# Kernel optimization log

Hardware: AMD Instinct MI355X
Metric: run time of the kernel (lower is better)

Reference implementation:

```python
import jax, jax.numpy as jnp
import numpy as np

B, N, D, H, P = 4, 512, 256, 8, 3
HD = D // H
EPS = 1e-5

def _ln(x, g, b):
    m = jnp.mean(x, axis=-1, keepdims=True)
    v = jnp.var(x, axis=-1, keepdims=True)
    return (x - m) * jax.lax.rsqrt(v + EPS) * g + b

def setup_inputs() -> dict:
    key = jax.random.key(0)
    ks = jax.random.split(key, 12)
    s = lambda *sh: 1.0 / np.sqrt(sh[0])
    return {
        "x": jax.random.normal(ks[0], (B, N, D), jnp.float32),
        "mask": jax.random.randint(ks[1], (B, N), 0, 2).astype(bool),
        "pair_feat": jax.random.normal(ks[2], (B, N, N, P), jnp.float32),
        "Wqkv": jax.random.normal(ks[3], (D, 3 * D), jnp.float32) * s(D),
        "Wout": jax.random.normal(ks[4], (D, D), jnp.float32) * s(D),
        "bout": jnp.zeros((D,), jnp.float32),
        "Wp1": jax.random.normal(ks[5], (P, D), jnp.float32) * s(P),
        "bp1": jnp.zeros((D,), jnp.float32),
        "Wp2": jax.random.normal(ks[6], (D, H), jnp.float32) * s(D),
        "bp2": jnp.zeros((H,), jnp.float32),
        "Wf1": jax.random.normal(ks[7], (D, 4 * D), jnp.float32) * s(D),
        "bf1": jnp.zeros((4 * D,), jnp.float32),
        "Wf2": jax.random.normal(ks[8], (4 * D, D), jnp.float32) * s(4 * D),
        "bf2": jnp.zeros((D,), jnp.float32),
        "g1": jnp.ones((D,), jnp.float32), "b1": jnp.zeros((D,), jnp.float32),
        "g2": jnp.ones((D,), jnp.float32), "b2": jnp.zeros((D,), jnp.float32),
    }

def reference(x, mask, pair_feat, Wqkv, Wout, bout, Wp1, bp1, Wp2, bp2,
              Wf1, bf1, Wf2, bf2, g1, b1, g2, b2):
    b_, n_, d_ = x.shape
    scale = HD ** -0.5
    qkv = x @ Wqkv                                  # [B,N,3D]
    q, k, v = jnp.split(qkv, 3, axis=-1)
    q = q.reshape(b_, n_, H, HD)
    k = k.reshape(b_, n_, H, HD)
    v = v.reshape(b_, n_, H, HD)
    logits = jnp.einsum('bihd,bjhd->bhij', q, k) * scale
    # pairwise bias MLP -> per-head bias [B,H,N,N]
    bias = jax.nn.relu(pair_feat @ Wp1 + bp1) @ Wp2 + bp2   # [B,N,N,H]
    logits = logits + jnp.transpose(bias, (0, 3, 1, 2))
    key_mask = ~mask[:, None, None, :]               # [B,1,1,N]
    logits = jnp.where(key_mask, -1e9, logits)
    attn = jax.nn.softmax(logits, axis=-1)
    out = jnp.einsum('bhij,bjhd->bihd', attn, v).reshape(b_, n_, d_)
    out = out @ Wout + bout
    x = _ln(x + out, g1, b1)
    h = jax.nn.gelu(x @ Wf1 + bf1, approximate=False) @ Wf2 + bf2
    return _ln(x + h, g2, b2)
```

## Files before the change

### kernel.cpp

```cpp
#include <hip/hip_runtime.h>
#include <hip/hip_fp16.h>
#include <math.h>

typedef unsigned short u16;
typedef short s16x8 __attribute__((ext_vector_type(8)));
typedef _Float16 f16x8 __attribute__((ext_vector_type(8)));
typedef float f32x4 __attribute__((ext_vector_type(4)));
typedef unsigned int u32x2 __attribute__((ext_vector_type(2)));

constexpr int CB = 4, CN = 512, CD = 256, CH = 8, CHD = 32;
constexpr float CEPS = 1e-5f;
constexpr int M_ROWS = CB * CN;
constexpr float QSCALE = 0.17677669529663687f;

constexpr size_t O_XB    = 0;
constexpr size_t O_QB    = 1048576;
constexpr size_t O_KB    = 2097152;
constexpr size_t O_VB    = 3145728;
constexpr size_t O_WQKVT = 4194304;
constexpr size_t O_WOUTT = O_WQKVT + 393216;
constexpr size_t O_WF1T  = O_WOUTT + 131072;
constexpr size_t O_WF2T  = O_WF1T + 524288;
constexpr size_t O_WP2T  = O_WF2T + 524288;
constexpr size_t O_PACKED= O_WP2T + 8192;
constexpr size_t O_JIDX  = O_PACKED + 4096;
constexpr size_t O_BIAS  = O_JIDX + 8192;
constexpr size_t O_AOUT  = O_BIAS + 16777216;
constexpr size_t O_H1B   = O_AOUT + 1048576;
constexpr size_t O_PRE1  = O_H1B + 4194304;
constexpr size_t O_PRE2  = O_PRE1 + 2097152;
constexpr size_t O_CNT   = O_PRE2 + 2097152;

__device__ inline u16 f2b(float f) {
  union { float f; unsigned u; } v{f};
  return (u16)((v.u + 0x7FFFu + ((v.u >> 16) & 1u)) >> 16);
}
__device__ inline float b2f(u16 b) {
  union { unsigned u; float f; } v{(unsigned)b << 16};
  return v.f;
}
__device__ inline f32x4 MFMA(s16x8 a, s16x8 b, f32x4 c) {
  return __builtin_amdgcn_mfma_f32_16x16x32_bf16(a, b, c, 0, 0, 0);
}
__device__ inline f32x4 MFMAH(f16x8 a, f16x8 b, f32x4 c) {
  return __builtin_amdgcn_mfma_f32_16x16x32_f16(a, b, c, 0, 0, 0);
}
__device__ inline unsigned cvtpk(float lo, float hi) {
  unsigned r;
  asm("v_cvt_pk_bf16_f32 %0, %1, %2" : "=v"(r) : "v"(lo), "v"(hi));
  return r;
}
__device__ inline unsigned pkmax0(unsigned a) {
  unsigned d;
  asm("v_pk_max_f16 %0, %1, 0" : "=v"(d) : "v"(a));
  return d;
}

__global__ __launch_bounds__(256) void prep_kernel(
    const float* __restrict__ x, const float* __restrict__ Wqkv,
    const float* __restrict__ Wout, const float* __restrict__ Wf1,
    const float* __restrict__ Wf2, const float* __restrict__ Wp2,
    const float* __restrict__ Wp1, const float* __restrict__ bp1,
    const unsigned char* __restrict__ maskraw,
    u16* __restrict__ xb, u16* __restrict__ wqkvt, u16* __restrict__ woutt,
    u16* __restrict__ wf1t, u16* __restrict__ wf2t, u16* __restrict__ wp2t,
    unsigned* __restrict__ packed, int* __restrict__ jidxg,
    int* __restrict__ cntg) {
  __shared__ int mode_max;
  __shared__ int mdec[2048];
  int blk = blockIdx.x, tid = threadIdx.x;
  if (blk < 256) {
    for (int t = tid; t < 512; t += 256) {
      float4 v = ((const float4*)x)[blk * 512 + t];
      u16 o0 = f2b(v.x), o1 = f2b(v.y), o2 = f2b(v.z), o3 = f2b(v.w);
      u32x2 w; w.x = (unsigned)o0 | ((unsigned)o1 << 16);
      w.y = (unsigned)o2 | ((unsigned)o3 << 16);
      *(u32x2*)(xb + (size_t)(blk * 512 + t) * 4) = w;
    }
  } else if (blk < 352) {
    int o0 = (blk - 256) * 2048;
    for (int t = tid; t < 2048; t += 256) {
      int o = o0 + t, n = o >> 8, k = o & 255;
      wqkvt[o] = f2b(Wqkv[k * 768 + n]);
    }
  } else if (blk < 384) {
    int o0 = (blk - 352) * 2048;
    for (int t = tid; t < 2048; t += 256) {
      int o = o0 + t, n = o >> 8, k = o & 255;
      woutt[o] = f2b(Wout[k * 256 + n]);
    }
  } else if (blk < 512) {
    int o0 = (blk - 384) * 2048;
    for (int t = tid; t < 2048; t += 256) {
      int o = o0 + t, n = o >> 8, k = o & 255;
      wf1t[o] = f2b(Wf1[k * 1024 + n]);
    }
  } else if (blk < 640) {
    int o0 = (blk - 512) * 2048;
    for (int t = tid; t < 2048; t += 256) {
      int o = o0 + t, n = o >> 10, k = o & 1023;
      wf2t[o] = f2b(Wf2[k * 256 + n]);
    }
  } else if (blk == 640) {
    for (int t = tid; t < 4096; t += 256) {
      int h = t >> 8, c = t & 255;
      wp2t[t] = (h < 8) ? __half_as_ushort(__float2half(Wp2[c * 8 + h])) : (u16)0;
    }
    if (tid < 128) {
      int p = tid * 2;
      unsigned w0 = (unsigned)__half_as_ushort(__float2half(Wp1[p]))
                  | ((unsigned)__half_as_ushort(__float2half(Wp1[p + 1])) << 16);
      unsigned w1 = (unsigned)__half_as_ushort(__float2half(Wp1[256 + p]))
                  | ((unsigned)__half_as_ushort(__float2half(Wp1[256 + p + 1])) << 16);
      unsigned w2 = (unsigned)__half_as_ushort(__float2half(Wp1[512 + p]))
                  | ((unsigned)__half_as_ushort(__float2half(Wp1[512 + p + 1])) << 16);
      unsigned bb = (unsigned)__half_as_ushort(__float2half(bp1[p]))
                  | ((unsigned)__half_as_ushort(__float2half(bp1[p + 1])) << 16);
      uint4 o; o.x = w0; o.y = w1; o.z = w2; o.w = bb;
      ((uint4*)packed)[tid] = o;
    }
  } else {
    if (tid == 0) mode_max = 0;
    __syncthreads();
    int lm = 0;
    for (int i = tid; i < CB*CN; i += 256)
      if ((i & 3) != 0) lm = max(lm, (int)maskraw[i]);
    atomicMax(&mode_max, lm);
    __syncthreads();
    int mv = mode_max;
    for (int i = tid; i < CB*CN; i += 256) {
      int val;
      if (mv == 0)      val = (((const int*)maskraw)[i] != 0);
      else if (mv == 1) val = (maskraw[i] != 0);
      else              val = (((const unsigned int*)maskraw)[i] != 0);
      mdec[i] = val;
    }
    __syncthreads();
    int w = tid >> 6, lane = tid & 63;
    if (w < 4) {
      int b = w, basei = 0;
      for (int c = 0; c < 8; ++c) {
        int j = c * 64 + lane;
        int m = mdec[b * 512 + j];
        unsigned long long bal = __ballot(m != 0);
        int off = __popcll(bal & ((1ull << lane) - 1ull));
        if (m) jidxg[b * 512 + basei + off] = j;
        basei += (int)__popcll(bal);
      }
      if (lane == 0) cntg[b] = basei;
      for (int p = basei + lane; p < 512; p += 64) jidxg[b * 512 + p] = 0;
    }
  }
}

__global__ __launch_bounds__(256) void qkv_pbias_kernel(
    const u16* __restrict__ A, const u16* __restrict__ Wt,
    u16* __restrict__ qb, u16* __restrict__ kb, u16* __restrict__ vb,
    const float* __restrict__ pf, const unsigned* __restrict__ packed,
    const u16* __restrict__ wp2t, const float* __restrict__ bp2,
    const int* __restrict__ jidxg, const int* __restrict__ cntg,
    u16* __restrict__ biasc) {
  __shared__ uint4 smem[1024];
  const int blk = blockIdx.x, tid = threadIdx.x;
  const int lane = tid & 63, w = tid >> 6;
  if (blk < 384) {
    u16* As = (u16*)smem;
    u16* Bs = (u16*)smem + 64 * 64;
    const int wm = w >> 1, wn = w & 1;
    const int bm = (blk / 12) * 64, bn = (blk % 12) * 64;
    f32x4 fz = {0.f, 0.f, 0.f, 0.f};
    f32x4 acc[2][2] = {{fz, fz}, {fz, fz}};
    for (int k0 = 0; k0 < 256; k0 += 64) {
#pragma unroll
      for (int t = tid; t < 512; t += 256) {
        int r = t >> 3, s = t & 7;
        s16x8 v = *(const s16x8*)(A + (size_t)(bm + r) * 256 + k0 + s * 8);
        *(s16x8*)(As + r * 64 + ((s ^ (r & 7)) << 3)) = v;
      }
#pragma unroll
      for (int t = tid; t < 512; t += 256) {
        int r = t >> 3, s = t & 7;
        s16x8 v = *(const s16x8*)(Wt + (size_t)(bn + r) * 256 + k0 + s * 8);
        *(s16x8*)(Bs + r * 64 + ((s ^ (r & 7)) << 3)) = v;
      }
      __syncthreads();
#pragma unroll
      for (int ks = 0; ks < 2; ++ks) {
        s16x8 af[2], bf[2];
#pragma unroll
        for (int mf = 0; mf < 2; ++mf) {
          int r = wm * 32 + mf * 16 + (lane & 15);
          int s = ks * 4 + (lane >> 4);
          af[mf] = *(const s16x8*)(As + r * 64 + ((s ^ (r & 7)) << 3));
        }
#pragma unroll
        for (int nf = 0; nf < 2; ++nf) {
          int r = wn * 32 + nf * 16 + (lane & 15);
          int s = ks * 4 + (lane >> 4);
          bf[nf] = *(const s16x8*)(Bs + r * 64 + ((s ^ (r & 7)) << 3));
        }
#pragma unroll
        for (int mf = 0; mf < 2; ++mf)
#pragma unroll
          for (int nf = 0; nf < 2; ++nf)
            acc[mf][nf] = MFMA(af[mf], bf[nf], acc[mf][nf]);
      }
      __syncthreads();
    }
#pragma unroll
    for (int mf = 0; mf < 2; ++mf) {
#pragma unroll
      for (int nf = 0; nf < 2; ++nf) {
#pragma unroll
        for (int r = 0; r < 4; ++r) {
          int m = bm + wm * 32 + mf * 16 + (lane >> 4) * 4 + r;
          int n = bn + wn * 32 + nf * 16 + (lane & 15);
          float v = acc[mf][nf][r];
          if (n < 256) {
            qb[(size_t)m * 256 + n] = f2b(v * QSCALE);
          } else if (n < 512) {
            kb[(size_t)m * 256 + (n - 256)] = f2b(v);
          } else {
            vb[(size_t)m * 256 + (n - 512)] = f2b(v);
          }
        }
      }
    }
  } else {
    uint4* pk = smem;
    float* pfl = (float*)(smem + 128);
    int* ji = (int*)(smem + 512);
    const int bid = blk - 384;
    const int b = bid >> 9, i = bid & 511;
    const int q = lane >> 4, hr = lane & 15;
    if (tid < 128) pk[tid] = ((const uint4*)packed)[tid];
    const float4* pfr = (const float4*)(pf + (size_t)(b * 512 + i) * 1536);
#pragma unroll
    for (int t = tid; t < 384; t += 256) ((float4*)pfl)[t] = pfr[t];
    for (int t = tid; t < 512; t += 256) ji[t] = jidxg[b * 512 + t];
    const int cnt = cntg[b];
    __syncthreads();
    __half2 f0d[8], f1d[8], f2d[8];
#pragma unroll
    for (int t = 0; t < 8; ++t) {
      int g = t * 4 + w;
      if (g * 16 < cnt) {
        int jsrc = ji[g * 16 + hr];
        f0d[t] = __float2half2_rn(pfl[jsrc * 3 + 0]);
        f1d[t] = __float2half2_rn(pfl[jsrc * 3 + 1]);
        f2d[t] = __float2half2_rn(pfl[jsrc * 3 + 2]);
      }
    }
    f32x4 fz = {0.f, 0.f, 0.f, 0.f};
    f32x4 acc[8] = {fz, fz, fz, fz, fz, fz, fz, fz};
    for (int chunk = 0; chunk < 8; ++chunk) {
      f16x8 wfrag = *(const f16x8*)(wp2t + hr * 256 + chunk * 32 + q * 8);
      int pbase = chunk * 16 + q * 4;
      __half2 w0[4], w1[4], w2[4], bb[4];
#pragma unroll
      for (int p = 0; p < 4; ++p) {
        uint4 c = pk[pbase + p];
        w0[p] = *(const __half2*)&c.x;
        w1[p] = *(const __half2*)&c.y;
        w2[p] = *(const __half2*)&c.z;
        bb[p] = *(const __half2*)&c.w;
      }
#pragma unroll
      for (int t = 0; t < 8; ++t) {
        int g = t * 4 + w;
        if (g * 16 < cnt) {
          union { unsigned u[4]; f16x8 v; } af;
#pragma unroll
          for (int p = 0; p < 4; ++p) {
            __half2 h = __hfma2(f0d[t], w0[p], bb[p]);
            h = __hfma2(f1d[t], w1[p], h);
            h = __hfma2(f2d[t], w2[p], h);
            af.u[p] = pkmax0(*(const unsigned*)&h);
          }
          acc[t] = MFMAH(af.v, wfrag, acc[t]);
        }
      }
    }
    if (hr < 8) {
      float bb = bp2[hr];
      size_t base = ((size_t)(b * 8 + hr) * 512 + i) * 512;
#pragma unroll
      for (int t = 0; t < 8; ++t) {
        int g = t * 4 + w;
        if (g * 16 < cnt) {
          int p0 = g * 16 + q * 4;
          u32x2 o;
          o.x = cvtpk(acc[t][0] + bb, acc[t][1] + bb);
          o.y = cvtpk(acc[t][2] + bb, acc[t][3] + bb);
          *(u32x2*)(biasc + base + p0) = o;
        }
      }
    }
  }
}

__global__ __launch_bounds__(512) void flash_kernel(
    const u16* __restrict__ qb, const u16* __restrict__ kb,
    const u16* __restrict__ vb, const u16* __restrict__ biasc,
    const int* __restrict__ jidxg, const int* __restrict__ cntg,
    u16* __restrict__ aout) {
  const int i0 = blockIdx.x * 64, h = blockIdx.y, b = blockIdx.z;
  const int tid = threadIdx.x;
  const int lane = tid & 63, w = tid >> 6;
  const int mf = w & 3, jhalf = w >> 2;
  __shared__ u16 qs[64 * 32];
  __shared__ u16 ksh[128 * 32];
  __shared__ u16 vs[32 * 128];
  __shared__ u16 ps[8][16 * 64];
  __shared__ float cmb[4][2][16][2];
  __shared__ int ji[512];
  for (int t = tid; t < 512; t += 512) ji[t] = jidxg[b * 512 + t];
  for (int t = tid; t < 256; t += 512) {
    int r = t >> 2, s = t & 3;
    s16x8 v = *(const s16x8*)(qb + (size_t)(b * 512 + i0 + r) * 256 + h * 32 + s * 8);
    *(s16x8*)(qs + r * 32 + ((s ^ (r & 3)) << 3)) = v;
  }
  const int cnt = cntg[b];
  __syncthreads();
  f32x4 fz = {0.f, 0.f, 0.f, 0.f};
  f32x4 oacc[2] = {fz, fz};
  float mrun[4] = {-3e38f, -3e38f, -3e38f, -3e38f};
  float lrun[4] = {0.f, 0.f, 0.f, 0.f};
  const int jj0 = jhalf * 64;
  const int il = mf * 16 + (lane >> 4) * 4;
  const u16* bbase = biasc + ((size_t)((b * 8 + h) * 512 + i0 + il)) * 512
                   + jj0 + (lane & 15);
  const int NJT = (cnt + 127) >> 7;
  for (int jc = 0; jc < NJT; ++jc) {
    int j0 = jc * 128;
    {
      int r = tid >> 2, s = tid & 3;
      int jsrc = ji[j0 + r];
      s16x8 v = *(const s16x8*)(kb + (size_t)(b * 512 + jsrc) * 256 + h * 32 + s * 8);
      *(s16x8*)(ksh + r * 32 + ((s ^ (r & 3)) << 3)) = v;
    }
    {
      int r = tid >> 2, s = tid & 3;
      int jsrc = ji[j0 + r];
      s16x8 v = *(const s16x8*)(vb + (size_t)(b * 512 + jsrc) * 256 + h * 32 + s * 8);
      int slot = r >> 3, el = r & 7;
#pragma unroll
      for (int e = 0; e < 8; ++e) {
        int d = s * 8 + e;
        vs[d * 128 + (((slot & 8) | ((slot & 7) ^ (d & 7))) << 3) + el] = (u16)v[e];
      }
    }
    u16 bvr[4][4];
#pragma unroll
    for (int jf = 0; jf < 4; ++jf)
#pragma unroll
      for (int r = 0; r < 4; ++r)
        bvr[jf][r] = bbase[(size_t)r * 512 + j0 + jf * 16];
    __syncthreads();
    int mk[4];
#pragma unroll
    for (int jf = 0; jf < 4; ++jf)
      mk[jf] = (j0 + jj0 + jf * 16 + (lane & 15)) < cnt;
    int arow = mf * 16 + (lane & 15);
    s16x8 af = *(const s16x8*)(qs + arow * 32 + (((lane >> 4) ^ (arow & 3)) << 3));
    f32x4 sm[4];
#pragma unroll
    for (int jf = 0; jf < 4; ++jf) {
      int brow = jj0 + jf * 16 + (lane & 15);
      s16x8 bfr = *(const s16x8*)(ksh + brow * 32 + (((lane >> 4) ^ (brow & 3)) << 3));
      sm[jf] = MFMA(af, bfr, fz);
    }
#pragma unroll
    for (int jf = 0; jf < 4; ++jf) {
#pragma unroll
      for (int r = 0; r < 4; ++r) {
        float sval = sm[jf][r] + b2f(bvr[jf][r]);
        sm[jf][r] = mk[jf] ? sval : -1e9f;
      }
    }
    float mx[4];
#pragma unroll
    for (int r = 0; r < 4; ++r)
      mx[r] = fmaxf(fmaxf(sm[0][r], sm[1][r]), fmaxf(sm[2][r], sm[3][r]));
#pragma unroll
    for (int d = 1; d < 16; d <<= 1)
#pragma unroll
      for (int r = 0; r < 4; ++r) mx[r] = fmaxf(mx[r], __shfl_xor(mx[r], d));
    float psl[4] = {0.f, 0.f, 0.f, 0.f};
#pragma unroll
    for (int jf = 0; jf < 4; ++jf)
#pragma unroll
      for (int r = 0; r < 4; ++r) {
        float p = __expf(sm[jf][r] - mx[r]);
        sm[jf][r] = p; psl[r] += p;
      }
#pragma unroll
    for (int d = 1; d < 16; d <<= 1)
#pragma unroll
      for (int r = 0; r < 4; ++r) psl[r] += __shfl_xor(psl[r], d);
    if ((lane & 15) == 0) {
#pragma unroll
      for (int r = 0; r < 4; ++r) {
        int row = (lane >> 4) * 4 + r;
        cmb[mf][jhalf][row][0] = mx[r];
        cmb[mf][jhalf][row][1] = psl[r];
      }
    }
    __syncthreads();
    float selfs[4];
#pragma unroll
    for (int r = 0; r < 4; ++r) {
      int row = (lane >> 4) * 4 + r;
      float omx = cmb[mf][1 - jhalf][row][0];
      float ops = cmb[mf][1 - jhalf][row][1];
      float tm = fmaxf(mx[r], omx);
      float nm = fmaxf(mrun[r], tm);
      float sc = __expf(mrun[r] - nm);
      selfs[r] = __expf(mx[r] - nm);
      float ptile = psl[r] * selfs[r] + ops * __expf(omx - nm);
      lrun[r] = lrun[r] * sc + ptile;
      mrun[r] = nm;
      oacc[0][r] *= sc; oacc[1][r] *= sc;
    }
    u16* pw = &ps[w][0];
#pragma unroll
    for (int jf = 0; jf < 4; ++jf) {
      int jcol = jf * 16 + (lane & 15);
      int slot = jcol >> 3, el = jcol & 7;
#pragma unroll
      for (int r = 0; r < 4; ++r) {
        int row = (lane >> 4) * 4 + r;
        pw[row * 64 + ((slot ^ (row & 7)) << 3) + el] = f2b(sm[jf][r] * selfs[r]);
      }
    }
#pragma unroll
    for (int kw = 0; kw < 2; ++kw) {
      int prow = lane & 15;
      s16x8 pa = *(const s16x8*)(pw + prow * 64 + (((kw * 4 + (lane >> 4)) ^ (prow & 7)) << 3));
#pragma unroll
      for (int df = 0; df < 2; ++df) {
        int drow = df * 16 + (lane & 15);
        int jcol = jj0 + kw * 32 + ((lane >> 4) << 3);
        int slot = jcol >> 3;
        s16x8 vv = *(const s16x8*)(vs + drow * 128 + (((slot & 8) | ((slot & 7) ^ (drow & 7))) << 3));
        oacc[df] = MFMA(pa, vv, oacc[df]);
      }
    }
    __syncthreads();
  }
  float* obuf = (float*)&ps[0][0];
  if (jhalf == 1) {
#pragma unroll
    for (int r = 0; r < 4; ++r) {
      int row = mf * 16 + (lane >> 4) * 4 + r;
#pragma unroll
      for (int df = 0; df < 2; ++df)
        obuf[row * 33 + df * 16 + (lane & 15)] = oacc[df][r];
    }
  }
  __syncthreads();
  if (jhalf == 0) {
#pragma unroll
    for (int r = 0; r < 4; ++r) {
      float inv = 1.0f / lrun[r];
      int row = mf * 16 + (lane >> 4) * 4 + r;
      int i = i0 + row;
#pragma unroll
      for (int df = 0; df < 2; ++df) {
        int d = df * 16 + (lane & 15);
        float o = (oacc[df][r] + obuf[row * 33 + d]) * inv;
        aout[(size_t)(b * 512 + i) * 256 + h * 32 + d] = f2b(o);
      }
    }
  }
}

__global__ __launch_bounds__(256) void mgemm_res(
    const u16* __restrict__ A, const u16* __restrict__ Wt,
    const float* __restrict__ bias, const float* __restrict__ R,
    float* __restrict__ outf, int N, int K) {
  __shared__ u16 As[32 * 64];
  __shared__ u16 Bs[64 * 64];
  const int tid = threadIdx.x;
  const int lane = tid & 63, w = tid >> 6;
  const int wm = w >> 1, wn = w & 1;
  const int bm = blockIdx.y * 32, bn = blockIdx.x * 64;
  f32x4 fz = {0.f, 0.f, 0.f, 0.f};
  f32x4 acc[2] = {fz, fz};
  for (int k0 = 0; k0 < K; k0 += 64) {
    for (int t = tid; t < 256; t += 256) {
      int r = t >> 3, s = t & 7;
      s16x8 v = *(const s16x8*)(A + (size_t)(bm + r) * K + k0 + s * 8);
      *(s16x8*)(As + r * 64 + ((s ^ (r & 7)) << 3)) = v;
    }
#pragma unroll
    for (int t = tid; t < 512; t += 256) {
      int r = t >> 3, s = t & 7;
      s16x8 v = *(const s16x8*)(Wt + (size_t)(bn + r) * K + k0 + s * 8);
      *(s16x8*)(Bs + r * 64 + ((s ^ (r & 7)) << 3)) = v;
    }
    __syncthreads();
#pragma unroll
    for (int ks = 0; ks < 2; ++ks) {
      int r = wm * 16 + (lane & 15);
      int s = ks * 4 + (lane >> 4);
      s16x8 af = *(const s16x8*)(As + r * 64 + ((s ^ (r & 7)) << 3));
#pragma unroll
      for (int nf = 0; nf < 2; ++nf) {
        int br = wn * 32 + nf * 16 + (lane & 15);
        s16x8 bf = *(const s16x8*)(Bs + br * 64 + ((s ^ (br & 7)) << 3));
        acc[nf] = MFMA(af, bf, acc[nf]);
      }
    }
    __syncthreads();
  }
#pragma unroll
  for (int nf = 0; nf < 2; ++nf) {
#pragma unroll
    for (int r = 0; r < 4; ++r) {
      int m = bm + wm * 16 + (lane >> 4) * 4 + r;
      int n = bn + wn * 32 + nf * 16 + (lane & 15);
      outf[(size_t)m * N + n] = acc[nf][r] + bias[n] + R[(size_t)m * N + n];
    }
  }
}

__global__ __launch_bounds__(256) void ffn1_kernel(
    const float* __restrict__ pre1, const u16* __restrict__ Wt,
    const float* __restrict__ bias, const float* __restrict__ g1,
    const float* __restrict__ b1, u16* __restrict__ outb) {
  __shared__ u16 As[64 * 64];
  __shared__ u16 Bs[64 * 64];
  __shared__ float rowm[64], rowr[64];
  const int tid = threadIdx.x;
  const int lane = tid & 63, w = tid >> 6;
  const int wm = w >> 1, wn = w & 1;
  const int bm = blockIdx.y * 64, bn = blockIdx.x * 64;
  {
    int r = tid >> 2, qd = tid & 3;
    const float4* pr = (const float4*)(pre1 + (size_t)(bm + r) * 256 + qd * 64);
    float s = 0.f, ss = 0.f;
#pragma unroll
    for (int u = 0; u < 16; ++u) {
      float4 v = pr[u];
      s += v.x + v.y + v.z + v.w;
      ss += v.x*v.x + v.y*v.y + v.z*v.z + v.w*v.w;
    }
    s += __shfl_xor(s, 1); ss += __shfl_xor(ss, 1);
    s += __shfl_xor(s, 2); ss += __shfl_xor(ss, 2);
    if (qd == 0) {
      float mean = s * (1.0f / 256.0f);
      float var  = ss * (1.0f / 256.0f) - mean * mean;
      rowm[r] = mean; rowr[r] = rsqrtf(var + CEPS);
    }
  }
  __syncthreads();
  f32x4 fz = {0.f, 0.f, 0.f, 0.f};
  f32x4 acc[2][2] = {{fz, fz}, {fz, fz}};
  for (int k0 = 0; k0 < 256; k0 += 64) {
#pragma unroll
    for (int t = tid; t < 512; t += 256) {
      int r = t >> 3, s = t & 7;
      float mean = rowm[r], rstd = rowr[r];
      const float4* pr = (const float4*)(pre1 + (size_t)(bm + r) * 256 + k0 + s * 8);
      float4 a0 = pr[0], a1 = pr[1];
      const float4* gp = (const float4*)(g1 + k0 + s * 8);
      const float4* bp = (const float4*)(b1 + k0 + s * 8);
      float4 g0 = gp[0], g1v = gp[1], c0 = bp[0], c1 = bp[1];
      union { unsigned u[4]; s16x8 v; } pk2;
      pk2.u[0] = cvtpk((a0.x-mean)*rstd*g0.x + c0.x, (a0.y-mean)*rstd*g0.y + c0.y);
      pk2.u[1] = cvtpk((a0.z-mean)*rstd*g0.z + c0.z, (a0.w-mean)*rstd*g0.w + c0.w);
      pk2.u[2] = cvtpk((a1.x-mean)*rstd*g1v.x + c1.x, (a1.y-mean)*rstd*g1v.y + c1.y);
      pk2.u[3] = cvtpk((a1.z-mean)*rstd*g1v.z + c1.z, (a1.w-mean)*rstd*g1v.w + c1.w);
      *(s16x8*)(As + r * 64 + ((s ^ (r & 7)) << 3)) = pk2.v;
    }
#pragma unroll
    for (int t = tid; t < 512; t += 256) {
      int r = t >> 3, s = t & 7;
      s16x8 v = *(const s16x8*)(Wt + (size_t)(bn + r) * 256 + k0 + s * 8);
      *(s16x8*)(Bs + r * 64 + ((s ^ (r & 7)) << 3)) = v;
    }
    __syncthreads();
#pragma unroll
    for (int ks = 0; ks < 2; ++ks) {
      s16x8 af[2], bf[2];
#pragma unroll
      for (int mf = 0; mf < 2; ++mf) {
        int r = wm * 32 + mf * 16 + (lane & 15);
        int s = ks * 4 + (lane >> 4);
        af[mf] = *(const s16x8*)(As + r * 64 + ((s ^ (r & 7)) << 3));
      }
#pragma unroll
      for (int nf = 0; nf < 2; ++nf) {
        int r = wn * 32 + nf * 16 + (lane & 15);
        int s = ks * 4 + (lane >> 4);
        bf[nf] = *(const s16x8*)(Bs + r * 64 + ((s ^ (r & 7)) << 3));
      }
#pragma unroll
      for (int mf = 0; mf < 2; ++mf)
#pragma unroll
        for (int nf = 0; nf < 2; ++nf)
          acc[mf][nf] = MFMA(af[mf], bf[nf], acc[mf][nf]);
    }
    __syncthreads();
  }
#pragma unroll
  for (int mf = 0; mf < 2; ++mf) {
#pragma unroll
    for (int nf = 0; nf < 2; ++nf) {
#pragma unroll
      for (int r = 0; r < 4; ++r) {
        int m = bm + wm * 32 + mf * 16 + (lane >> 4) * 4 + r;
        int n = bn + wn * 32 + nf * 16 + (lane & 15);
        float gv = acc[mf][nf][r] + bias[n];
        gv = 0.5f * gv * (1.0f + erff(gv * 0.70710678118654752f));
        outb[(size_t)m * 1024 + n] = f2b(gv);
      }
    }
  }
}

__global__ __launch_bounds__(256) void ffn2_kernel(
    const u16* __restrict__ A, const u16* __restrict__ Wt,
    const float* __restrict__ bias, const float* __restrict__ pre1,
    const float* __restrict__ g1, const float* __restrict__ b1,
    float* __restrict__ outf) {
  __shared__ u16 As[32 * 64];
  __shared__ u16 Bs[64 * 64];
  __shared__ float rowm[32], rowr[32];
  const int tid = threadIdx.x;
  const int lane = tid & 63, w = tid >> 6;
  const int wm = w >> 1, wn = w & 1;
  const int bm = blockIdx.y * 32, bn = blockIdx.x * 64;
  {
    int r = tid >> 3, od = tid & 7;
    const float4* pr = (const float4*)(pre1 + (size_t)(bm + r) * 256 + od * 32);
    float s = 0.f, ss = 0.f;
#pragma unroll
    for (int u = 0; u < 8; ++u) {
      float4 v = pr[u];
      s += v.x + v.y + v.z + v.w;
      ss += v.x*v.x + v.y*v.y + v.z*v.z + v.w*v.w;
    }
    s += __shfl_xor(s, 1); ss += __shfl_xor(ss, 1);
    s += __shfl_xor(s, 2); ss += __shfl_xor(ss, 2);
    s += __shfl_xor(s, 4); ss += __shfl_xor(ss, 4);
    if (od == 0) {
      float mean = s * (1.0f / 256.0f);
      float var  = ss * (1.0f / 256.0f) - mean * mean;
      rowm[r] = mean; rowr[r] = rsqrtf(var + CEPS);
    }
  }
  __syncthreads();
  f32x4 fz = {0.f, 0.f, 0.f, 0.f};
  f32x4 acc[2] = {fz, fz};
  for (int k0 = 0; k0 < 1024; k0 += 64) {
    for (int t = tid; t < 256; t += 256) {
      int r = t >> 3, s = t & 7;
      s16x8 v = *(const s16x8*)(A + (size_t)(bm + r) * 1024 + k0 + s * 8);
      *(s16x8*)(As + r * 64 + ((s ^ (r & 7)) << 3)) = v;
    }
#pragma unroll
    for (int t = tid; t < 512; t += 256) {
      int r = t >> 3, s = t & 7;
      s16x8 v = *(const s16x8*)(Wt + (size_t)(bn + r) * 1024 + k0 + s * 8);
      *(s16x8*)(Bs + r * 64 + ((s ^ (r & 7)) << 3)) = v;
    }
    __syncthreads();
#pragma unroll
    for (int ks = 0; ks < 2; ++ks) {
      int r = wm * 16 + (lane & 15);
      int s = ks * 4 + (lane >> 4);
      s16x8 af = *(const s16x8*)(As + r * 64 + ((s ^ (r & 7)) << 3));
#pragma unroll
      for (int nf = 0; nf < 2; ++nf) {
        int br = wn * 32 + nf * 16 + (lane & 15);
        s16x8 bf = *(const s16x8*)(Bs + br * 64 + ((s ^ (br & 7)) << 3));
        acc[nf] = MFMA(af, bf, acc[nf]);
      }
    }
    __syncthreads();
  }
#pragma unroll
  for (int nf = 0; nf < 2; ++nf) {
#pragma unroll
    for (int r = 0; r < 4; ++r) {
      int m = bm + wm * 16 + (lane >> 4) * 4 + r;
      int n = bn + wn * 32 + nf * 16 + (lane & 15);
      float mean = rowm[m - bm], rstd = rowr[m - bm];
      float xr = (pre1[(size_t)m * 256 + n] - mean) * rstd * g1[n] + b1[n];
      outf[(size_t)m * 256 + n] = acc[nf][r] + bias[n] + xr;
    }
  }
}

__global__ __launch_bounds__(256) void ln_kernel(
    const float* __restrict__ in, const float* __restrict__ g,
    const float* __restrict__ be, float* __restrict__ op) {
  int row = blockIdx.x * 4 + (threadIdx.x >> 6);
  int lane = threadIdx.x & 63;
  const float* x = in + (size_t)row * CD;
  float4 v = *(const float4*)&x[lane * 4];
  float s  = v.x + v.y + v.z + v.w;
  float ss = v.x*v.x + v.y*v.y + v.z*v.z + v.w*v.w;
#pragma unroll
  for (int off = 32; off > 0; off >>= 1) {
    s  += __shfl_xor(s, off);
    ss += __shfl_xor(ss, off);
  }
  float mean = s * (1.0f / CD);
  float var  = ss * (1.0f / CD) - mean * mean;
  float inv  = rsqrtf(var + CEPS);
  float4 gg = *(const float4*)&g[lane * 4];
  float4 bb = *(const float4*)&be[lane * 4];
  float4 o;
  o.x = (v.x - mean) * inv * gg.x + bb.x;
  o.y = (v.y - mean) * inv * gg.y + bb.y;
  o.z = (v.z - mean) * inv * gg.z + bb.z;
  o.w = (v.w - mean) * inv * gg.w + bb.w;
  *(float4*)&op[(size_t)row * CD + lane * 4] = o;
}

extern "C" void kernel_launch(void* const* d_in, const int* in_sizes, int n_in,
                              void* d_out, int out_size, void* d_ws, size_t ws_size,
                              hipStream_t stream) {
  (void)in_sizes; (void)n_in; (void)out_size; (void)ws_size;
  const float* x    = (const float*)d_in[0];
  const void*  mask = d_in[1];
  const float* pf   = (const float*)d_in[2];
  const float* Wqkv = (const float*)d_in[3];
  const float* Wout = (const float*)d_in[4];
  const float* bout = (const float*)d_in[5];
  const float* Wp1  = (const float*)d_in[6];
  const float* bp1  = (const float*)d_in[7];
  const float* Wp2  = (const float*)d_in[8];
  const float* bp2  = (const float*)d_in[9];
  const float* Wf1  = (const float*)d_in[10];
  const float* bf1  = (const float*)d_in[11];
  const float* Wf2  = (const float*)d_in[12];
  const float* bf2  = (const float*)d_in[13];
  const float* g1   = (const float*)d_in[14];
  const float* b1   = (const float*)d_in[15];
  const float* g2   = (const float*)d_in[16];
  const float* b2   = (const float*)d_in[17];

  char* ws = (char*)d_ws;
  u16* xb     = (u16*)(ws + O_XB);
  u16* qb     = (u16*)(ws + O_QB);
  u16* kb     = (u16*)(ws + O_KB);
  u16* vb     = (u16*)(ws + O_VB);
  u16* wqkvt  = (u16*)(ws + O_WQKVT);
  u16* woutt  = (u16*)(ws + O_WOUTT);
  u16* wf1t   = (u16*)(ws + O_WF1T);
  u16* wf2t   = (u16*)(ws + O_WF2T);
  u16* wp2t   = (u16*)(ws + O_WP2T);
  unsigned* packed = (unsigned*)(ws + O_PACKED);
  int* jidxg  = (int*)(ws + O_JIDX);
  int* cntg   = (int*)(ws + O_CNT);
  u16* biasc  = (u16*)(ws + O_BIAS);
  u16* aout   = (u16*)(ws + O_AOUT);
  u16* h1b    = (u16*)(ws + O_H1B);
  float* pre1 = (float*)(ws + O_PRE1);
  float* pre2 = (float*)(ws + O_PRE2);
  float* out  = (float*)d_out;

  hipLaunchKernelGGL(prep_kernel, dim3(642), dim3(256), 0, stream,
                     x, Wqkv, Wout, Wf1, Wf2, Wp2, Wp1, bp1,
                     (const unsigned char*)mask,
                     xb, wqkvt, woutt, wf1t, wf2t, wp2t, packed, jidxg, cntg);
  hipLaunchKernelGGL(qkv_pbias_kernel, dim3(2432), dim3(256), 0, stream,
                     xb, wqkvt, qb, kb, vb,
                     pf, packed, wp2t, bp2, jidxg, cntg, biasc);
  hipLaunchKernelGGL(flash_kernel, dim3(8, 8, 4), dim3(512), 0, stream,
                     qb, kb, vb, biasc, jidxg, cntg, aout);
  hipLaunchKernelGGL(mgemm_res, dim3(4, 64), dim3(256), 0, stream,
                     aout, woutt, bout, x, pre1, 256, 256);
  hipLaunchKernelGGL(ffn1_kernel, dim3(16, 32), dim3(256), 0, stream,
                     pre1, wf1t, bf1, g1, b1, h1b);
  hipLaunchKernelGGL(ffn2_kernel, dim3(4, 64), dim3(256), 0, stream,
                     h1b, wf2t, bf2, pre1, g1, b1, pre2);
  hipLaunchKernelGGL(ln_kernel, dim3(M_ROWS / 4), dim3(256), 0, stream,
                     pre2, g2, b2, out);
}
```

Before: 96.68 us.

## Store V pre-transposed and mask-compacted; move weight prep into qkv kernel

The QKV GEMM epilogue now writes V in a per-head transposed layout with key positions compacted by the mask, using a new inverse-position table built in the prep kernel. The flash kernel can then load V tiles with contiguous 16-byte loads and vector LDS stores instead of gathering rows and scattering elements. The Wout/Wf1/Wf2 transposes move from the prep kernel into extra blocks of the QKV kernel, shortening the prep kernel that sits on the critical path. The cost is scattered 2-byte global writes in the QKV epilogue.

```diff
diff --git a/kernel.cpp b/kernel.cpp
--- a/kernel.cpp
+++ b/kernel.cpp
@@ -16,7 +16,7 @@
 constexpr size_t O_XB    = 0;
 constexpr size_t O_QB    = 1048576;
 constexpr size_t O_KB    = 2097152;
-constexpr size_t O_VB    = 3145728;
+constexpr size_t O_VT    = 3145728;
 constexpr size_t O_WQKVT = 4194304;
 constexpr size_t O_WOUTT = O_WQKVT + 393216;
 constexpr size_t O_WF1T  = O_WOUTT + 131072;
@@ -30,6 +30,7 @@
 constexpr size_t O_PRE1  = O_H1B + 4194304;
 constexpr size_t O_PRE2  = O_PRE1 + 2097152;
 constexpr size_t O_CNT   = O_PRE2 + 2097152;
+constexpr size_t O_IPOS  = O_CNT + 256;
 
 __device__ inline u16 f2b(float f) {
   union { float f; unsigned u; } v{f};
@@ -58,14 +59,12 @@
 
 __global__ __launch_bounds__(256) void prep_kernel(
     const float* __restrict__ x, const float* __restrict__ Wqkv,
-    const float* __restrict__ Wout, const float* __restrict__ Wf1,
-    const float* __restrict__ Wf2, const float* __restrict__ Wp2,
+    const float* __restrict__ Wp2,
     const float* __restrict__ Wp1, const float* __restrict__ bp1,
     const unsigned char* __restrict__ maskraw,
-    u16* __restrict__ xb, u16* __restrict__ wqkvt, u16* __restrict__ woutt,
-    u16* __restrict__ wf1t, u16* __restrict__ wf2t, u16* __restrict__ wp2t,
+    u16* __restrict__ xb, u16* __restrict__ wqkvt, u16* __restrict__ wp2t,
     unsigned* __restrict__ packed, int* __restrict__ jidxg,
-    int* __restrict__ cntg) {
+    int* __restrict__ cntg, int* __restrict__ iposg) {
   __shared__ int mode_max;
   __shared__ int mdec[2048];
   int blk = blockIdx.x, tid = threadIdx.x;
@@ -83,25 +82,7 @@
       int o = o0 + t, n = o >> 8, k = o & 255;
       wqkvt[o] = f2b(Wqkv[k * 768 + n]);
     }
-  } else if (blk < 384) {
-    int o0 = (blk - 352) * 2048;
-    for (int t = tid; t < 2048; t += 256) {
-      int o = o0 + t, n = o >> 8, k = o & 255;
-      woutt[o] = f2b(Wout[k * 256 + n]);
-    }
-  } else if (blk < 512) {
-    int o0 = (blk - 384) * 2048;
-    for (int t = tid; t < 2048; t += 256) {
-      int o = o0 + t, n = o >> 8, k = o & 255;
-      wf1t[o] = f2b(Wf1[k * 1024 + n]);
-    }
-  } else if (blk < 640) {
-    int o0 = (blk - 512) * 2048;
-    for (int t = tid; t < 2048; t += 256) {
-      int o = o0 + t, n = o >> 10, k = o & 1023;
-      wf2t[o] = f2b(Wf2[k * 256 + n]);
-    }
-  } else if (blk == 640) {
+  } else if (blk == 352) {
     for (int t = tid; t < 4096; t += 256) {
       int h = t >> 8, c = t & 255;
       wp2t[t] = (h < 8) ? __half_as_ushort(__float2half(Wp2[c * 8 + h])) : (u16)0;
@@ -138,14 +119,19 @@
     __syncthreads();
     int w = tid >> 6, lane = tid & 63;
     if (w < 4) {
-      int b = w, basei = 0;
+      int b = w, basei = 0, basem = 0;
       for (int c = 0; c < 8; ++c) {
         int j = c * 64 + lane;
         int m = mdec[b * 512 + j];
         unsigned long long bal = __ballot(m != 0);
-        int off = __popcll(bal & ((1ull << lane) - 1ull));
-        if (m) jidxg[b * 512 + basei + off] = j;
+        int off  = __popcll(bal & ((1ull << lane) - 1ull));
+        int offm = __popcll(~bal & ((1ull << lane) - 1ull));
+        int pos;
+        if (m) { pos = basei + off; jidxg[b * 512 + pos] = j; }
+        else   { pos = 511 - (basem + offm); }
+        iposg[b * 512 + j] = pos;
         basei += (int)__popcll(bal);
+        basem += (int)(64 - __popcll(bal));
       }
       if (lane == 0) cntg[b] = basei;
       for (int p = basei + lane; p < 512; p += 64) jidxg[b * 512 + p] = 0;
@@ -155,11 +141,14 @@
 
 __global__ __launch_bounds__(256) void qkv_pbias_kernel(
     const u16* __restrict__ A, const u16* __restrict__ Wt,
-    u16* __restrict__ qb, u16* __restrict__ kb, u16* __restrict__ vb,
+    u16* __restrict__ qb, u16* __restrict__ kb, u16* __restrict__ vt,
     const float* __restrict__ pf, const unsigned* __restrict__ packed,
     const u16* __restrict__ wp2t, const float* __restrict__ bp2,
     const int* __restrict__ jidxg, const int* __restrict__ cntg,
-    u16* __restrict__ biasc) {
+    const int* __restrict__ iposg, u16* __restrict__ biasc,
+    const float* __restrict__ Wout, const float* __restrict__ Wf1,
+    const float* __restrict__ Wf2, u16* __restrict__ woutt,
+    u16* __restrict__ wf1t, u16* __restrict__ wf2t) {
   __shared__ uint4 smem[1024];
   const int blk = blockIdx.x, tid = threadIdx.x;
   const int lane = tid & 63, w = tid >> 6;
@@ -221,12 +210,15 @@
           } else if (n < 512) {
             kb[(size_t)m * 256 + (n - 256)] = f2b(v);
           } else {
-            vb[(size_t)m * 256 + (n - 512)] = f2b(v);
+            int nv = n - 512, h = nv >> 5, d = nv & 31;
+            int bb = m >> 9, j = m & 511;
+            int pos = iposg[bb * 512 + j];
+            vt[(size_t)((bb * 8 + h) * 32 + d) * 512 + pos] = f2b(v);
           }
         }
       }
     }
-  } else {
+  } else if (blk < 2432) {
     uint4* pk = smem;
     float* pfl = (float*)(smem + 128);
     int* ji = (int*)(smem + 512);
@@ -296,12 +288,30 @@
         }
       }
     }
+  } else if (blk < 2464) {
+    int o0 = (blk - 2432) * 2048;
+    for (int t = tid; t < 2048; t += 256) {
+      int o = o0 + t, n = o >> 8, k = o & 255;
+      woutt[o] = f2b(Wout[k * 256 + n]);
+    }
+  } else if (blk < 2592) {
+    int o0 = (blk - 2464) * 2048;
+    for (int t = tid; t < 2048; t += 256) {
+      int o = o0 + t, n = o >> 8, k = o & 255;
+      wf1t[o] = f2b(Wf1[k * 1024 + n]);
+    }
+  } else {
+    int o0 = (blk - 2592) * 2048;
+    for (int t = tid; t < 2048; t += 256) {
+      int o = o0 + t, n = o >> 10, k = o & 1023;
+      wf2t[o] = f2b(Wf2[k * 256 + n]);
+    }
   }
 }
 
 __global__ __launch_bounds__(512) void flash_kernel(
     const u16* __restrict__ qb, const u16* __restrict__ kb,
-    const u16* __restrict__ vb, const u16* __restrict__ biasc,
+    const u16* __restrict__ vt, const u16* __restrict__ biasc,
     const int* __restrict__ jidxg, const int* __restrict__ cntg,
     u16* __restrict__ aout) {
   const int i0 = blockIdx.x * 64, h = blockIdx.y, b = blockIdx.z;
@@ -340,15 +350,9 @@
       *(s16x8*)(ksh + r * 32 + ((s ^ (r & 3)) << 3)) = v;
     }
     {
-      int r = tid >> 2, s = tid & 3;
-      int jsrc = ji[j0 + r];
-      s16x8 v = *(const s16x8*)(vb + (size_t)(b * 512 + jsrc) * 256 + h * 32 + s * 8);
-      int slot = r >> 3, el = r & 7;
-#pragma unroll
-      for (int e = 0; e < 8; ++e) {
-        int d = s * 8 + e;
-        vs[d * 128 + (((slot & 8) | ((slot & 7) ^ (d & 7))) << 3) + el] = (u16)v[e];
-      }
+      int r = tid >> 4, s = tid & 15;
+      s16x8 v = *(const s16x8*)(vt + (size_t)((b * 8 + h) * 32 + r) * 512 + j0 + s * 8);
+      *(s16x8*)(vs + r * 128 + (((s & 8) | ((s & 7) ^ (r & 7))) << 3)) = v;
     }
     u16 bvr[4][4];
 #pragma unroll
@@ -748,7 +752,7 @@
   u16* xb     = (u16*)(ws + O_XB);
   u16* qb     = (u16*)(ws + O_QB);
   u16* kb     = (u16*)(ws + O_KB);
-  u16* vb     = (u16*)(ws + O_VB);
+  u16* vt     = (u16*)(ws + O_VT);
   u16* wqkvt  = (u16*)(ws + O_WQKVT);
   u16* woutt  = (u16*)(ws + O_WOUTT);
   u16* wf1t   = (u16*)(ws + O_WF1T);
@@ -757,6 +761,7 @@
   unsigned* packed = (unsigned*)(ws + O_PACKED);
   int* jidxg  = (int*)(ws + O_JIDX);
   int* cntg   = (int*)(ws + O_CNT);
+  int* iposg  = (int*)(ws + O_IPOS);
   u16* biasc  = (u16*)(ws + O_BIAS);
   u16* aout   = (u16*)(ws + O_AOUT);
   u16* h1b    = (u16*)(ws + O_H1B);
@@ -764,15 +769,16 @@
   float* pre2 = (float*)(ws + O_PRE2);
   float* out  = (float*)d_out;
 
-  hipLaunchKernelGGL(prep_kernel, dim3(642), dim3(256), 0, stream,
-                     x, Wqkv, Wout, Wf1, Wf2, Wp2, Wp1, bp1,
+  hipLaunchKernelGGL(prep_kernel, dim3(354), dim3(256), 0, stream,
+                     x, Wqkv, Wp2, Wp1, bp1,
                      (const unsigned char*)mask,
-                     xb, wqkvt, woutt, wf1t, wf2t, wp2t, packed, jidxg, cntg);
-  hipLaunchKernelGGL(qkv_pbias_kernel, dim3(2432), dim3(256), 0, stream,
-                     xb, wqkvt, qb, kb, vb,
-                     pf, packed, wp2t, bp2, jidxg, cntg, biasc);
+                     xb, wqkvt, wp2t, packed, jidxg, cntg, iposg);
+  hipLaunchKernelGGL(qkv_pbias_kernel, dim3(2720), dim3(256), 0, stream,
+                     xb, wqkvt, qb, kb, vt,
+                     pf, packed, wp2t, bp2, jidxg, cntg, iposg, biasc,
+                     Wout, Wf1, Wf2, woutt, wf1t, wf2t);
   hipLaunchKernelGGL(flash_kernel, dim3(8, 8, 4), dim3(512), 0, stream,
-                     qb, kb, vb, biasc, jidxg, cntg, aout);
+                     qb, kb, vt, biasc, jidxg, cntg, aout);
   hipLaunchKernelGGL(mgemm_res, dim3(4, 64), dim3(256), 0, stream,
                      aout, woutt, bout, x, pre1, 256, 256);
   hipLaunchKernelGGL(ffn1_kernel, dim3(16, 32), dim3(256), 0, stream,
```

After: 95.37 us, median of 2. About the same (-1.4%).
